# Performance work log

Measured on AMD Instinct MI355X. Metric: run time of the kernel, lower is better.

Reference implementation:

```python
import jax, jax.numpy as jnp
import numpy as np

N_NODES = 100000
N_EDGES = 3200000
D_FEAT = 512
D_HID = 64
D_LAT = 16
N_CLASS = 10
N_FLOW = 10
K_PROP = 10
ALPHA_TELEPORT = 0.1


def setup_inputs() -> dict:
    key = jax.random.key(0)
    ks = jax.random.split(key, 8)
    x = jax.random.normal(ks[0], (N_NODES, D_FEAT), jnp.float32)
    edge_index = jax.random.randint(ks[1], (2, N_EDGES), 0, N_NODES)
    p_c = jax.random.uniform(ks[2], (N_CLASS,), jnp.float32) + 0.1
    p_c = p_c / p_c.sum()
    W1 = jax.random.normal(ks[3], (D_FEAT, D_HID), jnp.float32) / np.sqrt(D_FEAT).astype(np.float32)
    b1 = jnp.zeros((D_HID,), jnp.float32)
    W2 = jax.random.normal(ks[4], (D_HID, D_LAT), jnp.float32) / np.sqrt(D_HID).astype(np.float32)
    b2 = jnp.zeros((D_LAT,), jnp.float32)
    flow_z0 = jax.random.normal(ks[5], (N_FLOW, N_CLASS, D_LAT), jnp.float32) * 0.1
    flow_alpha_prime = jax.random.normal(ks[6], (N_FLOW, N_CLASS, 1), jnp.float32) * 0.1
    flow_beta = jax.random.normal(ks[7], (N_FLOW, N_CLASS, 1), jnp.float32) * 0.1
    return dict(x=x, edge_index=edge_index, p_c=p_c, W1=W1, b1=b1, W2=W2, b2=b2,
                flow_z0=flow_z0, flow_alpha_prime=flow_alpha_prime, flow_beta=flow_beta)


def _batched_radial_log_prob(z, flow_z0, flow_alpha_prime, flow_beta):
    # Per-class batched radial flow (invertible pyro-style parameterization).
    # z: [N, D] -> log_q: [N, C]
    C, D = flow_z0.shape[1], flow_z0.shape[2]
    zz = jnp.broadcast_to(z[None], (C, z.shape[0], D))  # [C, N, D]
    sum_logdet = jnp.zeros((C, z.shape[0]), z.dtype)
    for l in range(flow_z0.shape[0]):  # small fixed number of flow layers
        z0 = flow_z0[l][:, None, :]                               # [C,1,D]
        alpha = jax.nn.softplus(flow_alpha_prime[l])[:, None, :]  # [C,1,1]
        beta_hat = -alpha + jax.nn.softplus(flow_beta[l])[:, None, :]
        dz = zz - z0
        r = jnp.sqrt(jnp.sum(dz * dz, axis=-1, keepdims=True))    # [C,N,1]
        h = 1.0 / (alpha + r)
        bh = beta_hat * h
        zz = zz + bh * dz
        logdet = (D - 1) * jnp.log1p(bh) + jnp.log1p(bh - beta_hat * r * h * h)
        sum_logdet = sum_logdet + logdet[..., 0]
    log_base = -0.5 * jnp.sum(zz * zz, axis=-1) - 0.5 * D * jnp.log(2.0 * jnp.pi)
    return (log_base + sum_logdet).T  # [N, C]


def _appnp(beta_ft, edge_index, n_nodes):
    # APPNP with self loops and symmetric gcn normalization over edge list.
    src = jnp.concatenate([edge_index[0], jnp.arange(n_nodes)])
    dst = jnp.concatenate([edge_index[1], jnp.arange(n_nodes)])
    deg = jax.ops.segment_sum(jnp.ones_like(src, dtype=beta_ft.dtype), dst, num_segments=n_nodes)
    dinv = jnp.where(deg > 0, jax.lax.rsqrt(jnp.maximum(deg, 1.0)), 0.0)
    norm = (dinv[src] * dinv[dst])[:, None]  # [E+N, 1]
    x0 = beta_ft
    b = beta_ft
    for _ in range(K_PROP):
        agg = jax.ops.segment_sum(norm * b[src], dst, num_segments=n_nodes)
        b = (1.0 - ALPHA_TELEPORT) * agg + ALPHA_TELEPORT * x0
    return b


def reference(x, edge_index, p_c, W1, b1, W2, b2, flow_z0, flow_alpha_prime, flow_beta):
    h = jax.nn.relu(x @ W1 + b1)           # input_encoder (dropout inactive at eval)
    z = h @ W2 + b2                        # latent_encoder, [N, D_LAT]
    log_q = _batched_radial_log_prob(z, flow_z0, flow_alpha_prime, flow_beta)
    log_q_per_class = log_q + jnp.log(p_c)[None, :]
    log_scale = 0.5 * D_LAT * jnp.log(4.0 * jnp.pi)  # 'latent-new' evidence scale
    beta_ft = jnp.exp(jnp.clip(log_q_per_class + log_scale, -30.0, 30.0))
    beta = _appnp(beta_ft, edge_index, x.shape[0])
    alpha = 1.0 + beta
    soft = alpha / jnp.sum(alpha, axis=-1, keepdims=True)
    hard = jnp.argmax(soft, axis=-1)
    return hard[:, None], soft
```

## Files before the change

### kernel.cpp

```cpp
#include <hip/hip_runtime.h>
#include <math.h>
#include <limits.h>

#define DF 512
#define DH 64
#define DL 16
#define NC 10
#define NF 10
#define KPROP 10

#define BSH 7
#define BW  (1 << BSH)
#define MAXB 1024
#define TILE 16384

__device__ __forceinline__ float softplus_(float x){
  return fmaxf(x, 0.0f) + log1pf(expf(-fabsf(x)));
}

#define BM 64
#define BN 64
#define BK 32
__global__ __launch_bounds__(256) void k_gemm1z(const float* __restrict__ x,
    const float* __restrict__ W1, const float* __restrict__ b1,
    const float* __restrict__ W2, const float* __restrict__ b2,
    float* __restrict__ z, int N)
{
  __shared__ float smem[2*BK*(BM+4)];
  float (*At)[BM+4] = (float(*)[BM+4])smem;
  float (*Bs)[BN+4] = (float(*)[BN+4])(smem + BK*(BM+4));
  __shared__ float W2s[DH][DL];
  __shared__ float b2s[DL];
  const int tid = threadIdx.x;
  for (int i = tid; i < DH*DL; i += 256) W2s[i>>4][i&15] = W2[i];
  if (tid < DL) b2s[tid] = b2[tid];
  const int tx = tid & 15, ty = tid >> 4;
  const int row0 = blockIdx.x * BM;
  float acc[4][4] = {};
  for (int k0 = 0; k0 < DF; k0 += BK) {
    #pragma unroll
    for (int i = 0; i < 2; ++i) {
      int idx = tid + i*256;
      int r  = idx >> 3;
      int kk = (idx & 7) << 2;
      int row = row0 + r;
      float4 va = make_float4(0.f,0.f,0.f,0.f);
      if (row < N) va = *(const float4*)&x[(size_t)row*DF + k0 + kk];
      At[kk+0][r]=va.x; At[kk+1][r]=va.y; At[kk+2][r]=va.z; At[kk+3][r]=va.w;
      int r2 = idx >> 4;
      int c4 = (idx & 15) << 2;
      float4 vb = *(const float4*)&W1[(size_t)(k0+r2)*DH + c4];
      Bs[r2][c4+0]=vb.x; Bs[r2][c4+1]=vb.y; Bs[r2][c4+2]=vb.z; Bs[r2][c4+3]=vb.w;
    }
    __syncthreads();
    #pragma unroll
    for (int kk = 0; kk < BK; ++kk) {
      float4 av = *(const float4*)&At[kk][ty<<2];
      float4 bv = *(const float4*)&Bs[kk][tx<<2];
      float a4[4]={av.x,av.y,av.z,av.w};
      float b4[4]={bv.x,bv.y,bv.z,bv.w};
      #pragma unroll
      for (int i=0;i<4;++i)
        #pragma unroll
        for (int j=0;j<4;++j) acc[i][j] = fmaf(a4[i], b4[j], acc[i][j]);
    }
    __syncthreads();
  }
  float4 bias = ((const float4*)b1)[tx];
  float bias4[4] = {bias.x, bias.y, bias.z, bias.w};
  float (*hs)[BM+4] = (float(*)[BM+4])smem;
  #pragma unroll
  for (int i=0;i<4;++i){
    #pragma unroll
    for (int j=0;j<4;++j)
      hs[(ty<<2)+i][(tx<<2)+j] = fmaxf(acc[i][j] + bias4[j], 0.0f);
  }
  __syncthreads();
  int row = tid >> 2, lg = tid & 3;
  float4 zacc = ((const float4*)b2s)[lg];
  #pragma unroll 8
  for (int k = 0; k < DH; ++k){
    float hv = hs[row][k];
    float4 wv = *(const float4*)&W2s[k][lg<<2];
    zacc.x = fmaf(hv, wv.x, zacc.x);
    zacc.y = fmaf(hv, wv.y, zacc.y);
    zacc.z = fmaf(hv, wv.z, zacc.z);
    zacc.w = fmaf(hv, wv.w, zacc.w);
  }
  int grow = row0 + row;
  if (grow < N) ((float4*)z)[(size_t)grow*4 + lg] = zacc;
}

__global__ __launch_bounds__(256) void k_flow2(const float* __restrict__ z,
    const float* __restrict__ pc, const float* __restrict__ z0g,
    const float* __restrict__ apg, const float* __restrict__ fbg,
    const float* __restrict__ dinv,
    float* __restrict__ x0, float* __restrict__ c0, float* __restrict__ y0, int N)
{
  __shared__ float z0s[NF][NC][DL];
  __shared__ float alps[NF][NC];
  __shared__ float bhs[NF][NC];
  __shared__ float lpc[NC];
  int tid = threadIdx.x;
  for (int i = tid; i < NF*NC*DL; i += 256)
    z0s[(i>>4)/NC][(i>>4)%NC][i&15] = z0g[i];
  if (tid < NF*NC){
    int l = tid/NC, c = tid%NC;
    float al = softplus_(apg[tid]);
    alps[l][c] = al;
    bhs[l][c]  = -al + softplus_(fbg[tid]);
  }
  if (tid < NC) lpc[tid] = __logf(pc[tid]);
  __syncthreads();

  int idx = blockIdx.x*256 + tid;
  int n = idx >> 4, c = idx & 15;
  if (n >= N) return;
  float dn = dinv[n];
  if (c >= NC){ x0[idx] = 0.f; c0[idx] = 0.f; y0[idx] = 0.f; return; }

  float zz[DL];
  const float4* z4 = (const float4*)z;
  #pragma unroll
  for (int q=0; q<4; ++q){
    float4 v = z4[(size_t)n*4 + q];
    zz[q*4+0]=v.x; zz[q*4+1]=v.y; zz[q*4+2]=v.z; zz[q*4+3]=v.w;
  }
  const float NEGHALFD_LOG2PI = -14.703016531274762f;
  const float LOGSCALE        =  20.248193975754326f;
  float sld = 0.f;
  #pragma unroll 1
  for (int l=0; l<NF; ++l){
    float al = alps[l][c], bhat = bhs[l][c];
    float dz[DL]; float r2 = 0.f;
    #pragma unroll
    for (int d=0; d<DL; ++d){ float t = zz[d] - z0s[l][c][d]; dz[d]=t; r2 = fmaf(t,t,r2); }
    float r  = sqrtf(r2);
    float hh = 1.0f/(al + r);
    float bh = bhat*hh;
    #pragma unroll
    for (int d=0; d<DL; ++d) zz[d] = fmaf(bh, dz[d], zz[d]);
    sld += 15.0f*__logf(1.0f + bh) + __logf(1.0f + bh - bhat*r*hh*hh);
  }
  float q2 = 0.f;
  #pragma unroll
  for (int d=0; d<DL; ++d) q2 = fmaf(zz[d], zz[d], q2);
  float v = -0.5f*q2 + NEGHALFD_LOG2PI + sld + lpc[c] + LOGSCALE;
  v = fminf(fmaxf(v, -30.f), 30.f);
  float xv = __expf(v);
  x0[idx] = xv;
  c0[idx] = dn*xv;
  y0[idx] = 0.1f*dn*xv;
}

__global__ __launch_bounds__(256) void k_bhist(const int* __restrict__ dst,
    int* __restrict__ bCnt, int E, int B)
{
  __shared__ int hh[MAXB];
  int tid = threadIdx.x;
  for (int b = tid; b < B; b += 256) hh[b] = 0;
  __syncthreads();
  for (int i = blockIdx.x*256 + tid; i < E; i += gridDim.x*256)
    atomicAdd(&hh[dst[i] >> BSH], 1);
  __syncthreads();
  for (int b = tid; b < B; b += 256) if (hh[b]) atomicAdd(&bCnt[b], hh[b]);
}

__global__ void k_bscan(const int* __restrict__ bCnt, int* __restrict__ bOff, int B){
  if (blockIdx.x==0 && threadIdx.x==0){
    int run = 0;
    for (int b=0;b<B;++b){ bOff[b]=run; run+=bCnt[b]; }
    bOff[B]=run;
  }
}

__global__ __launch_bounds__(256) void k_bscatter(const int* __restrict__ src,
    const int* __restrict__ dst, const int* __restrict__ bOff,
    int* __restrict__ bCur, int* __restrict__ bp, int E, int B)
{
  __shared__ int hc[MAXB];
  __shared__ int hb[MAXB];
  int tid = threadIdx.x;
  int base = blockIdx.x * TILE;
  int lim  = base + TILE; if (lim > E) lim = E;
  for (int b = tid; b < B; b += 256) hc[b] = 0;
  __syncthreads();
  for (int i = base + tid; i < lim; i += 256)
    atomicAdd(&hc[dst[i] >> BSH], 1);
  __syncthreads();
  for (int b = tid; b < B; b += 256){
    int c = hc[b];
    hb[b] = c ? atomicAdd(&bCur[b], c) : 0;
    hc[b] = 0;
  }
  __syncthreads();
  for (int i = base + tid; i < lim; i += 256){
    int d = dst[i];
    int b = d >> BSH;
    int pos = bOff[b] + hb[b] + atomicAdd(&hc[b], 1);
    bp[pos] = (src[i] << BSH) | (d & (BW-1));
  }
}

__global__ __launch_bounds__(256) void k_bdeg(const int* __restrict__ bp,
    const int* __restrict__ bOff, int* __restrict__ deg, int N)
{
  __shared__ int cur[BW];
  int tid = threadIdx.x;
  int b = blockIdx.x;
  if (tid < BW) cur[tid] = 0;
  __syncthreads();
  int s = bOff[b], e = bOff[b+1];
  for (int i = s + tid; i < e; i += 256)
    atomicAdd(&cur[bp[i] & (BW-1)], 1);
  __syncthreads();
  int node = (b << BSH) + tid;
  if (tid < BW && node < N) deg[node] = cur[tid] + 1;
}

__global__ void k_dinv(const int* __restrict__ deg, float* __restrict__ dinv,
    float* __restrict__ dinv2, int N){
  int n = blockIdx.x*256 + threadIdx.x;
  if (n < N){
    float d = (float)deg[n];
    float dv = 1.0f / sqrtf(d);
    dinv[n]  = dv;
    dinv2[n] = dv*dv;
  }
}

__global__ __launch_bounds__(256) void k_scan_part(const int* __restrict__ deg,
    int* __restrict__ part, int N){
  __shared__ int sd[256];
  int base = blockIdx.x*1024;
  int tid = threadIdx.x;
  int s = 0;
  #pragma unroll
  for (int i=0;i<4;++i){ int idx = base + tid*4 + i; if (idx < N) s += deg[idx]; }
  sd[tid] = s; __syncthreads();
  for (int ofs=128; ofs>0; ofs>>=1){ if (tid<ofs) sd[tid]+=sd[tid+ofs]; __syncthreads(); }
  if (tid==0) part[blockIdx.x] = sd[0];
}

__global__ void k_scan_top(int* part, int nb){
  if (blockIdx.x==0 && threadIdx.x==0){
    int run = 0;
    for (int i=0;i<nb;++i){ int v = part[i]; part[i] = run; run += v; }
  }
}

__global__ __launch_bounds__(256) void k_scan_final(const int* __restrict__ deg,
    const int* __restrict__ part, int* __restrict__ off, int N, int E)
{
  __shared__ int sc[256];
  int base = blockIdx.x*1024;
  int tid = threadIdx.x;
  int v[4]; int s = 0;
  #pragma unroll
  for (int i=0;i<4;++i){ int idx = base + tid*4 + i; v[i] = (idx<N)?deg[idx]:0; s += v[i]; }
  sc[tid] = s; __syncthreads();
  for (int ofs=1; ofs<256; ofs<<=1){
    int t = (tid>=ofs) ? sc[tid-ofs] : 0;
    __syncthreads();
    sc[tid] += t;
    __syncthreads();
  }
  int ex = sc[tid] - s + part[blockIdx.x];
  #pragma unroll
  for (int i=0;i<4;++i){
    int idx = base + tid*4 + i;
    if (idx < N){
      off[idx] = ex;
      if (idx == N-1) off[N] = ex + v[i];
      ex += v[i];
    }
  }
}

__global__ __launch_bounds__(256) void k_place(const int* __restrict__ bp,
    const int* __restrict__ bOff, const int* __restrict__ off,
    int* __restrict__ csr, int N)
{
  __shared__ int cur[BW];
  int tid = threadIdx.x;
  int b = blockIdx.x;
  int node0 = b << BSH;
  if (tid < BW){
    cur[tid] = 1;
    int node = node0 + tid;
    if (node < N) csr[off[node]] = node;
  }
  __syncthreads();
  int s = bOff[b], e = bOff[b+1];
  for (int i = s + tid; i < e; i += 256){
    int v  = bp[i];
    int dl = v & (BW-1);
    int sn = v >> BSH;
    int d  = node0 + dl;
    int p  = off[d] + atomicAdd(&cur[dl], 1);
    csr[p] = sn;
  }
}

__global__ __launch_bounds__(256) void k_rank(int* __restrict__ csr,
    const int* __restrict__ off, int N)
{
  int wid  = (blockIdx.x*256 + threadIdx.x) >> 6;
  int lane = threadIdx.x & 63;
  if (wid >= N) return;
  int s = off[wid], e = off[wid+1];
  int d = e - s;
  if (d <= 1) return;
  if (d <= 64){
    int v = (lane < d) ? csr[s+lane] : INT_MAX;
    int rank = 0;
    for (int j = 0; j < d; ++j){
      int bv = __shfl(v, j);
      rank += (bv < v) || (bv == v && j < lane);
    }
    if (lane < d) csr[s+rank] = v;
  } else if (d <= 256){
    int v0 = (lane      < d) ? csr[s+lane      ] : INT_MAX;
    int v1 = (lane+64   < d) ? csr[s+lane+64   ] : INT_MAX;
    int v2 = (lane+128  < d) ? csr[s+lane+128  ] : INT_MAX;
    int v3 = (lane+192  < d) ? csr[s+lane+192  ] : INT_MAX;
    int r0=0,r1=0,r2=0,r3=0;
    for (int j = 0; j < d; ++j){
      int slot = j >> 6, jl = j & 63;
      int bv = (slot==0) ? __shfl(v0,jl) : (slot==1) ? __shfl(v1,jl)
             : (slot==2) ? __shfl(v2,jl) : __shfl(v3,jl);
      r0 += (bv < v0) || (bv == v0 && j < lane);
      r1 += (bv < v1) || (bv == v1 && j < lane+64);
      r2 += (bv < v2) || (bv == v2 && j < lane+128);
      r3 += (bv < v3) || (bv == v3 && j < lane+192);
    }
    if (lane      < d) csr[s+r0]=v0;
    if (lane+64   < d) csr[s+r1]=v1;
    if (lane+128  < d) csr[s+r2]=v2;
    if (lane+192  < d) csr[s+r3]=v3;
  } else {
    if (lane == 0){
      for (int i = s+1; i < e; ++i){
        int key = csr[i]; int j = i-1;
        while (j >= s && csr[j] > key){ csr[j+1] = csr[j]; --j; }
        csr[j+1] = key;
      }
    }
  }
}

__global__ __launch_bounds__(256) void k_prop(const float* __restrict__ cin,
    const float* __restrict__ y0, const float* __restrict__ dinv2,
    float* __restrict__ cout,
    const int* __restrict__ csr, const int* __restrict__ off, int N)
{
  int t = blockIdx.x*256 + threadIdx.x;
  int n = t >> 2, q = t & 3;
  if (n >= N) return;
  const float4* c4 = (const float4*)cin;
  float4 a0 = make_float4(0.f,0.f,0.f,0.f);
  float4 a1 = make_float4(0.f,0.f,0.f,0.f);
  float4 a2 = make_float4(0.f,0.f,0.f,0.f);
  float4 a3 = make_float4(0.f,0.f,0.f,0.f);
  int s = off[n], e = off[n+1];
  int i = s;
  for (; i+4 <= e; i += 4){
    int s0 = csr[i], s1 = csr[i+1], s2 = csr[i+2], s3 = csr[i+3];
    float4 v0 = c4[(size_t)s0*4 + q];
    float4 v1 = c4[(size_t)s1*4 + q];
    float4 v2 = c4[(size_t)s2*4 + q];
    float4 v3 = c4[(size_t)s3*4 + q];
    a0.x += v0.x; a0.y += v0.y; a0.z += v0.z; a0.w += v0.w;
    a1.x += v1.x; a1.y += v1.y; a1.z += v1.z; a1.w += v1.w;
    a2.x += v2.x; a2.y += v2.y; a2.z += v2.z; a2.w += v2.w;
    a3.x += v3.x; a3.y += v3.y; a3.z += v3.z; a3.w += v3.w;
  }
  for (; i < e; ++i){
    float4 v0 = c4[(size_t)csr[i]*4 + q];
    a0.x += v0.x; a0.y += v0.y; a0.z += v0.z; a0.w += v0.w;
  }
  float w9 = 0.9f * dinv2[n];
  float4 yv = ((const float4*)y0)[(size_t)n*4 + q];
  float4 o;
  o.x = fmaf(w9, (a0.x+a1.x)+(a2.x+a3.x), yv.x);
  o.y = fmaf(w9, (a0.y+a1.y)+(a2.y+a3.y), yv.y);
  o.z = fmaf(w9, (a0.z+a1.z)+(a2.z+a3.z), yv.z);
  o.w = fmaf(w9, (a0.w+a1.w)+(a2.w+a3.w), yv.w);
  ((float4*)cout)[(size_t)n*4 + q] = o;
}

__global__ __launch_bounds__(256) void k_prop_final(const float* __restrict__ cin,
    const float* __restrict__ x0, const float* __restrict__ dinv,
    const int* __restrict__ csr, const int* __restrict__ off,
    float* __restrict__ out, int N)
{
  int t = blockIdx.x*256 + threadIdx.x;
  int n = t >> 2, q = t & 3;
  if (n >= N) return;
  const float4* c4 = (const float4*)cin;
  float4 a0 = make_float4(0.f,0.f,0.f,0.f);
  float4 a1 = make_float4(0.f,0.f,0.f,0.f);
  float4 a2 = make_float4(0.f,0.f,0.f,0.f);
  float4 a3 = make_float4(0.f,0.f,0.f,0.f);
  int s = off[n], e = off[n+1];
  int i = s;
  for (; i+4 <= e; i += 4){
    int s0 = csr[i], s1 = csr[i+1], s2 = csr[i+2], s3 = csr[i+3];
    float4 v0 = c4[(size_t)s0*4 + q];
    float4 v1 = c4[(size_t)s1*4 + q];
    float4 v2 = c4[(size_t)s2*4 + q];
    float4 v3 = c4[(size_t)s3*4 + q];
    a0.x += v0.x; a0.y += v0.y; a0.z += v0.z; a0.w += v0.w;
    a1.x += v1.x; a1.y += v1.y; a1.z += v1.z; a1.w += v1.w;
    a2.x += v2.x; a2.y += v2.y; a2.z += v2.z; a2.w += v2.w;
    a3.x += v3.x; a3.y += v3.y; a3.z += v3.z; a3.w += v3.w;
  }
  for (; i < e; ++i){
    float4 v0 = c4[(size_t)csr[i]*4 + q];
    a0.x += v0.x; a0.y += v0.y; a0.z += v0.z; a0.w += v0.w;
  }
  float w9 = 0.9f * dinv[n];
  float4 xv = ((const float4*)x0)[(size_t)n*4 + q];
  float4 al;
  al.x = fmaf(w9, (a0.x+a1.x)+(a2.x+a3.x), fmaf(0.1f, xv.x, 1.f));
  al.y = fmaf(w9, (a0.y+a1.y)+(a2.y+a3.y), fmaf(0.1f, xv.y, 1.f));
  al.z = fmaf(w9, (a0.z+a1.z)+(a2.z+a3.z), fmaf(0.1f, xv.z, 1.f));
  al.w = fmaf(w9, (a0.w+a1.w)+(a2.w+a3.w), fmaf(0.1f, xv.w, 1.f));

  float sv = 0.f;
  if (q < 2)       sv = al.x + al.y + al.z + al.w;
  else if (q == 2) sv = al.x + al.y;
  sv += __shfl_xor(sv, 1, 4);
  sv += __shfl_xor(sv, 2, 4);

  float bv = -1e30f; int bi = 999;
  int cb = q*4;
  int nvalid = (q < 2) ? 4 : (q == 2 ? 2 : 0);
  float av[4] = {al.x, al.y, al.z, al.w};
  for (int j = 0; j < nvalid; ++j){
    if (av[j] > bv){ bv = av[j]; bi = cb + j; }
  }
  #pragma unroll
  for (int o = 1; o <= 2; o <<= 1){
    float vo = __shfl_xor(bv, o, 4);
    int  io  = __shfl_xor(bi, o, 4);
    if (vo > bv || (vo == bv && io < bi)){ bv = vo; bi = io; }
  }

  float inv = 1.0f / sv;
  size_t sb = (size_t)N + (size_t)n*NC;
  for (int j = 0; j < nvalid; ++j) out[sb + cb + j] = av[j] * inv;
  if (q == 0) out[n] = (float)bi;
}

extern "C" void kernel_launch(void* const* d_in, const int* in_sizes, int n_in,
                              void* d_out, int out_size, void* d_ws, size_t ws_size,
                              hipStream_t stream)
{
  const float* x  = (const float*)d_in[0];
  const int*   ei = (const int*)  d_in[1];
  const float* pc = (const float*)d_in[2];
  const float* W1 = (const float*)d_in[3];
  const float* b1 = (const float*)d_in[4];
  const float* W2 = (const float*)d_in[5];
  const float* b2 = (const float*)d_in[6];
  const float* z0 = (const float*)d_in[7];
  const float* ap = (const float*)d_in[8];
  const float* fb = (const float*)d_in[9];
  float* out = (float*)d_out;

  const int N = in_sizes[0] / DF;
  const int E = in_sizes[1] / 2;
  const int* src = ei;
  const int* dst = ei + E;
  const int B = (N + BW - 1) >> BSH;

  char* ws = (char*)d_ws;
  size_t o = 0;
  size_t region0 = (size_t)E*sizeof(int);
  if ((size_t)N*DL*sizeof(float) > region0) region0 = (size_t)N*DL*sizeof(float);
  int*   bp   = (int*)  (ws + o);
  float* z    = (float*)(ws + o);
  o += region0;
  int*   csr  = (int*)  (ws + o); o += (size_t)(E+N)*sizeof(int);
  float* x0   = (float*)(ws + o); o += (size_t)N*DL*sizeof(float);
  float* c0   = (float*)(ws + o); o += (size_t)N*DL*sizeof(float);
  float* y0   = (float*)(ws + o); o += (size_t)N*DL*sizeof(float);
  float* cA   = (float*)(ws + o); o += (size_t)N*DL*sizeof(float);
  float* cB   = (float*)(ws + o); o += (size_t)N*DL*sizeof(float);
  int*   deg  = (int*)  (ws + o); o += (size_t)N*sizeof(int);
  float* dinv = (float*)(ws + o); o += (size_t)N*sizeof(float);
  float* dinv2= (float*)(ws + o); o += (size_t)N*sizeof(float);
  int*   offs = (int*)  (ws + o); o += (size_t)(N+2)*sizeof(int);
  int*   part = (int*)  (ws + o); o += 4096;
  int*   bCnt = (int*)  (ws + o); o += MAXB*sizeof(int);
  int*   bOff = (int*)  (ws + o); o += (MAXB+1)*sizeof(int);
  int*   bCur = (int*)  (ws + o); o += MAXB*sizeof(int);

  const int TB = 256;
  int gN  = (N + TB - 1) / TB;
  int nb  = (N + 1023) / 1024;

  hipMemsetAsync(bCnt, 0, MAXB*sizeof(int), stream);
  hipMemsetAsync(bCur, 0, MAXB*sizeof(int), stream);
  k_bhist<<<512, TB, 0, stream>>>(dst, bCnt, E, B);
  k_bscan<<<1, 1, 0, stream>>>(bCnt, bOff, B);
  k_bscatter<<<(E + TILE - 1)/TILE, TB, 0, stream>>>(src, dst, bOff, bCur, bp, E, B);
  k_bdeg<<<B, TB, 0, stream>>>(bp, bOff, deg, N);
  k_dinv<<<gN, TB, 0, stream>>>(deg, dinv, dinv2, N);
  k_scan_part<<<nb, TB, 0, stream>>>(deg, part, N);
  k_scan_top<<<1, 1, 0, stream>>>(part, nb);
  k_scan_final<<<nb, TB, 0, stream>>>(deg, part, offs, N, E);
  k_place<<<B, TB, 0, stream>>>(bp, bOff, offs, csr, N);
  k_rank<<<(N + 3) / 4, TB, 0, stream>>>(csr, offs, N);

  k_gemm1z<<<(N + BM - 1) / BM, TB, 0, stream>>>(x, W1, b1, W2, b2, z, N);
  k_flow2<<<((N*DL) + TB - 1) / TB, TB, 0, stream>>>(z, pc, z0, ap, fb, dinv,
                                                     x0, c0, y0, N);

  int gP = ((N*4) + TB - 1) / TB;
  const float* cin = c0;
  for (int it = 0; it < KPROP-1; ++it){
    float* cout = (it & 1) ? cB : cA;
    k_prop<<<gP, TB, 0, stream>>>(cin, y0, dinv2, cout, csr, offs, N);
    cin = cout;
  }
  k_prop_final<<<gP, TB, 0, stream>>>(cin, x0, dinv, csr, offs, out, N);
}
```

Measured before the change: 776.5 us.

## Retile encoder GEMM to 8x8 per-thread, fuse dinv into degree kernel, unroll prop

The input-encoder GEMM moves to 128-row tiles, 128 threads, 8x8 register tiles and BK=16. The second (W2) projection is now computed from registers, with shuffle reductions across 8 lanes instead of a shared-memory staging pass. The separate dinv kernel is folded into the per-bucket degree kernel, removing one launch and one pass over the degree array. The propagation gather loop gains an 8-way unrolled stage so more loads are in flight per thread. The larger per-thread tile raises register pressure and lowers occupancy, and each x row load is now strided per thread rather than coalesced.

New measurement: 870.8 us. 12.2% more time.

```diff
diff --git a/kernel.cpp b/kernel.cpp
--- a/kernel.cpp
+++ b/kernel.cpp
@@ -18,77 +18,108 @@
   return fmaxf(x, 0.0f) + log1pf(expf(-fabsf(x)));
 }
 
-#define BM 64
-#define BN 64
-#define BK 32
-__global__ __launch_bounds__(256) void k_gemm1z(const float* __restrict__ x,
+#define BM 128
+#define BKK 16
+__global__ __launch_bounds__(128) void k_gemm1z(const float* __restrict__ x,
     const float* __restrict__ W1, const float* __restrict__ b1,
     const float* __restrict__ W2, const float* __restrict__ b2,
     float* __restrict__ z, int N)
 {
-  __shared__ float smem[2*BK*(BM+4)];
-  float (*At)[BM+4] = (float(*)[BM+4])smem;
-  float (*Bs)[BN+4] = (float(*)[BN+4])(smem + BK*(BM+4));
-  __shared__ float W2s[DH][DL];
+  __shared__ float At[BKK][132];
+  __shared__ float Bs[BKK][68];
+  __shared__ float W2s[DH][17];
   __shared__ float b2s[DL];
   const int tid = threadIdx.x;
-  for (int i = tid; i < DH*DL; i += 256) W2s[i>>4][i&15] = W2[i];
+  for (int i = tid; i < DH*DL; i += 128){ W2s[i>>4][i&15] = W2[i]; }
   if (tid < DL) b2s[tid] = b2[tid];
-  const int tx = tid & 15, ty = tid >> 4;
+  const int tx = tid & 7, ty = tid >> 3;
   const int row0 = blockIdx.x * BM;
-  float acc[4][4] = {};
-  for (int k0 = 0; k0 < DF; k0 += BK) {
-    #pragma unroll
-    for (int i = 0; i < 2; ++i) {
-      int idx = tid + i*256;
-      int r  = idx >> 3;
-      int kk = (idx & 7) << 2;
-      int row = row0 + r;
+  const int myrow = row0 + tid;
+  const bool rowok = (myrow < N);
+  const float* xr = x + (size_t)(rowok ? myrow : 0) * DF;
+
+  float acc[8][8] = {};
+  for (int k0 = 0; k0 < DF; k0 += BKK){
+    #pragma unroll
+    for (int j = 0; j < 4; ++j){
       float4 va = make_float4(0.f,0.f,0.f,0.f);
-      if (row < N) va = *(const float4*)&x[(size_t)row*DF + k0 + kk];
-      At[kk+0][r]=va.x; At[kk+1][r]=va.y; At[kk+2][r]=va.z; At[kk+3][r]=va.w;
-      int r2 = idx >> 4;
-      int c4 = (idx & 15) << 2;
-      float4 vb = *(const float4*)&W1[(size_t)(k0+r2)*DH + c4];
-      Bs[r2][c4+0]=vb.x; Bs[r2][c4+1]=vb.y; Bs[r2][c4+2]=vb.z; Bs[r2][c4+3]=vb.w;
+      if (rowok) va = *(const float4*)&xr[k0 + j*4];
+      At[j*4+0][tid] = va.x; At[j*4+1][tid] = va.y;
+      At[j*4+2][tid] = va.z; At[j*4+3][tid] = va.w;
+    }
+    #pragma unroll
+    for (int j = 0; j < 2; ++j){
+      int idx = tid + j*128;
+      int kk = idx >> 4, c4 = (idx & 15) << 2;
+      float4 vb = *(const float4*)&W1[(size_t)(k0+kk)*DH + c4];
+      *(float4*)&Bs[kk][c4] = vb;
     }
     __syncthreads();
     #pragma unroll
-    for (int kk = 0; kk < BK; ++kk) {
-      float4 av = *(const float4*)&At[kk][ty<<2];
-      float4 bv = *(const float4*)&Bs[kk][tx<<2];
-      float a4[4]={av.x,av.y,av.z,av.w};
-      float b4[4]={bv.x,bv.y,bv.z,bv.w};
+    for (int kk = 0; kk < BKK; ++kk){
+      float4 a0 = *(const float4*)&At[kk][ty*8];
+      float4 a1 = *(const float4*)&At[kk][ty*8+4];
+      float4 b0 = *(const float4*)&Bs[kk][tx*8];
+      float4 b1v= *(const float4*)&Bs[kk][tx*8+4];
+      float a8[8] = {a0.x,a0.y,a0.z,a0.w,a1.x,a1.y,a1.z,a1.w};
+      float b8[8] = {b0.x,b0.y,b0.z,b0.w,b1v.x,b1v.y,b1v.z,b1v.w};
       #pragma unroll
-      for (int i=0;i<4;++i)
+      for (int i=0;i<8;++i)
         #pragma unroll
-        for (int j=0;j<4;++j) acc[i][j] = fmaf(a4[i], b4[j], acc[i][j]);
+        for (int j=0;j<8;++j) acc[i][j] = fmaf(a8[i], b8[j], acc[i][j]);
     }
     __syncthreads();
   }
-  float4 bias = ((const float4*)b1)[tx];
-  float bias4[4] = {bias.x, bias.y, bias.z, bias.w};
-  float (*hs)[BM+4] = (float(*)[BM+4])smem;
-  #pragma unroll
-  for (int i=0;i<4;++i){
-    #pragma unroll
-    for (int j=0;j<4;++j)
-      hs[(ty<<2)+i][(tx<<2)+j] = fmaxf(acc[i][j] + bias4[j], 0.0f);
-  }
-  __syncthreads();
-  int row = tid >> 2, lg = tid & 3;
-  float4 zacc = ((const float4*)b2s)[lg];
-  #pragma unroll 8
-  for (int k = 0; k < DH; ++k){
-    float hv = hs[row][k];
-    float4 wv = *(const float4*)&W2s[k][lg<<2];
-    zacc.x = fmaf(hv, wv.x, zacc.x);
-    zacc.y = fmaf(hv, wv.y, zacc.y);
-    zacc.z = fmaf(hv, wv.z, zacc.z);
-    zacc.w = fmaf(hv, wv.w, zacc.w);
-  }
-  int grow = row0 + row;
-  if (grow < N) ((float4*)z)[(size_t)grow*4 + lg] = zacc;
+
+  float4 bv0 = *(const float4*)&b1[tx*8];
+  float4 bv1 = *(const float4*)&b1[tx*8+4];
+  float bb[8] = {bv0.x,bv0.y,bv0.z,bv0.w,bv1.x,bv1.y,bv1.z,bv1.w};
+  #pragma unroll
+  for (int i=0;i<8;++i)
+    #pragma unroll
+    for (int j=0;j<8;++j) acc[i][j] = fmaxf(acc[i][j] + bb[j], 0.0f);
+
+  #pragma unroll
+  for (int b = 0; b < 4; ++b){
+    float zp[2][16];
+    #pragma unroll
+    for (int rr=0; rr<2; ++rr)
+      #pragma unroll
+      for (int c=0; c<16; ++c) zp[rr][c] = 0.f;
+    #pragma unroll
+    for (int j=0; j<8; ++j){
+      int c = tx*8 + j;
+      float w2r[16];
+      #pragma unroll
+      for (int zc=0; zc<16; ++zc) w2r[zc] = W2s[c][zc];
+      float h0 = acc[b*2+0][j], h1 = acc[b*2+1][j];
+      #pragma unroll
+      for (int zc=0; zc<16; ++zc){
+        zp[0][zc] = fmaf(h0, w2r[zc], zp[0][zc]);
+        zp[1][zc] = fmaf(h1, w2r[zc], zp[1][zc]);
+      }
+    }
+    #pragma unroll
+    for (int rr=0; rr<2; ++rr){
+      #pragma unroll
+      for (int zc=0; zc<16; ++zc){
+        float v = zp[rr][zc];
+        v += __shfl_xor(v, 1, 8);
+        v += __shfl_xor(v, 2, 8);
+        v += __shfl_xor(v, 4, 8);
+        zp[rr][zc] = v + b2s[zc];
+      }
+      int grow = row0 + ty*8 + b*2 + rr;
+      if (tx < 4 && grow < N){
+        float4 o;
+        if      (tx == 0) o = make_float4(zp[rr][0], zp[rr][1], zp[rr][2], zp[rr][3]);
+        else if (tx == 1) o = make_float4(zp[rr][4], zp[rr][5], zp[rr][6], zp[rr][7]);
+        else if (tx == 2) o = make_float4(zp[rr][8], zp[rr][9], zp[rr][10],zp[rr][11]);
+        else              o = make_float4(zp[rr][12],zp[rr][13],zp[rr][14],zp[rr][15]);
+        ((float4*)z)[(size_t)grow*4 + tx] = o;
+      }
+    }
+  }
 }
 
 __global__ __launch_bounds__(256) void k_flow2(const float* __restrict__ z,
@@ -203,7 +234,8 @@
 }
 
 __global__ __launch_bounds__(256) void k_bdeg(const int* __restrict__ bp,
-    const int* __restrict__ bOff, int* __restrict__ deg, int N)
+    const int* __restrict__ bOff, int* __restrict__ deg,
+    float* __restrict__ dinv, float* __restrict__ dinv2, int N)
 {
   __shared__ int cur[BW];
   int tid = threadIdx.x;
@@ -215,17 +247,12 @@
     atomicAdd(&cur[bp[i] & (BW-1)], 1);
   __syncthreads();
   int node = (b << BSH) + tid;
-  if (tid < BW && node < N) deg[node] = cur[tid] + 1;
-}
-
-__global__ void k_dinv(const int* __restrict__ deg, float* __restrict__ dinv,
-    float* __restrict__ dinv2, int N){
-  int n = blockIdx.x*256 + threadIdx.x;
-  if (n < N){
-    float d = (float)deg[n];
-    float dv = 1.0f / sqrtf(d);
-    dinv[n]  = dv;
-    dinv2[n] = dv*dv;
+  if (tid < BW && node < N){
+    int d = cur[tid] + 1;
+    deg[node] = d;
+    float dv = 1.0f / sqrtf((float)d);
+    dinv[node]  = dv;
+    dinv2[node] = dv*dv;
   }
 }
 
@@ -364,6 +391,26 @@
   float4 a3 = make_float4(0.f,0.f,0.f,0.f);
   int s = off[n], e = off[n+1];
   int i = s;
+  for (; i+8 <= e; i += 8){
+    int s0 = csr[i],   s1 = csr[i+1], s2 = csr[i+2], s3 = csr[i+3];
+    int s4 = csr[i+4], s5 = csr[i+5], s6 = csr[i+6], s7 = csr[i+7];
+    float4 v0 = c4[(size_t)s0*4 + q];
+    float4 v1 = c4[(size_t)s1*4 + q];
+    float4 v2 = c4[(size_t)s2*4 + q];
+    float4 v3 = c4[(size_t)s3*4 + q];
+    float4 v4 = c4[(size_t)s4*4 + q];
+    float4 v5 = c4[(size_t)s5*4 + q];
+    float4 v6 = c4[(size_t)s6*4 + q];
+    float4 v7 = c4[(size_t)s7*4 + q];
+    a0.x += v0.x; a0.y += v0.y; a0.z += v0.z; a0.w += v0.w;
+    a1.x += v1.x; a1.y += v1.y; a1.z += v1.z; a1.w += v1.w;
+    a2.x += v2.x; a2.y += v2.y; a2.z += v2.z; a2.w += v2.w;
+    a3.x += v3.x; a3.y += v3.y; a3.z += v3.z; a3.w += v3.w;
+    a0.x += v4.x; a0.y += v4.y; a0.z += v4.z; a0.w += v4.w;
+    a1.x += v5.x; a1.y += v5.y; a1.z += v5.z; a1.w += v5.w;
+    a2.x += v6.x; a2.y += v6.y; a2.z += v6.z; a2.w += v6.w;
+    a3.x += v7.x; a3.y += v7.y; a3.z += v7.z; a3.w += v7.w;
+  }
   for (; i+4 <= e; i += 4){
     int s0 = csr[i], s1 = csr[i+1], s2 = csr[i+2], s3 = csr[i+3];
     float4 v0 = c4[(size_t)s0*4 + q];
@@ -498,7 +545,6 @@
   int*   bCur = (int*)  (ws + o); o += MAXB*sizeof(int);
 
   const int TB = 256;
-  int gN  = (N + TB - 1) / TB;
   int nb  = (N + 1023) / 1024;
 
   hipMemsetAsync(bCnt, 0, MAXB*sizeof(int), stream);
@@ -506,15 +552,14 @@
   k_bhist<<<512, TB, 0, stream>>>(dst, bCnt, E, B);
   k_bscan<<<1, 1, 0, stream>>>(bCnt, bOff, B);
   k_bscatter<<<(E + TILE - 1)/TILE, TB, 0, stream>>>(src, dst, bOff, bCur, bp, E, B);
-  k_bdeg<<<B, TB, 0, stream>>>(bp, bOff, deg, N);
-  k_dinv<<<gN, TB, 0, stream>>>(deg, dinv, dinv2, N);
+  k_bdeg<<<B, TB, 0, stream>>>(bp, bOff, deg, dinv, dinv2, N);
   k_scan_part<<<nb, TB, 0, stream>>>(deg, part, N);
   k_scan_top<<<1, 1, 0, stream>>>(part, nb);
   k_scan_final<<<nb, TB, 0, stream>>>(deg, part, offs, N, E);
   k_place<<<B, TB, 0, stream>>>(bp, bOff, offs, csr, N);
   k_rank<<<(N + 3) / 4, TB, 0, stream>>>(csr, offs, N);
 
-  k_gemm1z<<<(N + BM - 1) / BM, TB, 0, stream>>>(x, W1, b1, W2, b2, z, N);
+  k_gemm1z<<<(N + BM - 1) / BM, 128, 0, stream>>>(x, W1, b1, W2, b2, z, N);
   k_flow2<<<((N*DL) + TB - 1) / TB, TB, 0, stream>>>(z, pc, z0, ap, fb, dinv,
                                                      x0, c0, y0, N);
 
```
